# Optimization experiments

Measured on AMD Instinct MI355X. Metric: run time of the kernel, lower is better.

The kernel has to match this reference:

```python
import jax, jax.numpy as jnp
import numpy as np

B, IC, H, W = 32, 128, 112, 112
OC, K, STRIDE, PAD = 256, 3, 2, 1


def setup_inputs() -> dict:
    key = jax.random.key(0)
    kx, kw = jax.random.split(key)
    x = jax.random.normal(kx, (B, IC, H, W), dtype=jnp.float32)
    weight = jax.random.normal(kw, (OC, IC, K, K), dtype=jnp.float32) * 0.01
    bias = jnp.zeros((OC,), dtype=jnp.float32)
    return {"x": x, "weight": weight, "bias": bias}


def reference(x, weight, bias):
    # Equivalent of the nested-loop conv: standard cross-correlation,
    # stride=2, zero padding=1, NCHW / OIHW layouts.
    out = jax.lax.conv_general_dilated(
        x, weight,
        window_strides=(STRIDE, STRIDE),
        padding=[(PAD, PAD), (PAD, PAD)],
        dimension_numbers=("NCHW", "OIHW", "NCHW"),
    )
    return out + bias[None, :, None, None]
```

## Files before the change

kernel.cpp:

```cpp
#include <hip/hip_runtime.h>
#include <hip/hip_bf16.h>


#define B_    32
#define IC_   128
#define H_    112
#define W_    112
#define HW_   (H_ * W_)
#define OC_   256
#define HP    113
#define NPIX  (B_ * 56 * 56)
#define XT_BYTES ((size_t)B_ * HP * HP * IC_ * 2)
#define WT2_BYTES ((size_t)36 * 16384)

typedef __attribute__((ext_vector_type(8))) short bf16x8;
typedef __attribute__((ext_vector_type(4))) float f32x4;

static __device__ __forceinline__ unsigned f2bf_u(float f) {
  union { float f; unsigned u; } v; v.f = f;
  return (v.u + 0x7FFF + ((v.u >> 16) & 1)) >> 16;
}

__global__ __launch_bounds__(256) void xtrans_kernel(
    const float* __restrict__ x, unsigned short* __restrict__ xt) {
  __shared__ unsigned short lds[128 * 128];
  const int ihp = blockIdx.x;
  const int b   = blockIdx.y;
  const int tid = threadIdx.x;

  if (ihp > 0) {
    const float* xp = x + (size_t)b * IC_ * HW_ + (size_t)(ihp - 1) * W_;
#pragma unroll
    for (int it = 0; it < 16; ++it) {
      const int i  = tid + it * 256;
      const int ic = i >> 5;
      const int g  = i & 31;
      if (g < 28) {
        const float4 v = *reinterpret_cast<const float4*>(
            xp + (size_t)ic * HW_ + g * 4);
        uint2 p;
        p.x = f2bf_u(v.x) | (f2bf_u(v.y) << 16);
        p.y = f2bf_u(v.z) | (f2bf_u(v.w) << 16);
        const int gs = g ^ (((ic >> 3) & 7) << 2);
        *reinterpret_cast<uint2*>(&lds[ic * 128 + gs * 4]) = p;
      }
    }
  }
  __syncthreads();

  unsigned short* xrow = xt + ((size_t)(b * HP + ihp)) * (HP * IC_);
  const bool live = (ihp > 0);
#pragma unroll
  for (int it = 0; it < 8; ++it) {
    const int e = tid + it * 256;
    if (e >= HP * 16) break;
    const int iwp = e >> 4;
    const int icg = e & 15;
    uint4 v = {0u, 0u, 0u, 0u};
    if (live && iwp > 0) {
      const int iw  = iwp - 1;
      const int col = ((iw >> 2) ^ ((icg & 7) << 2)) * 4 + (iw & 3);
      const int r0  = icg * 8;
      unsigned u0 = lds[(r0 + 0) * 128 + col];
      unsigned u1 = lds[(r0 + 1) * 128 + col];
      unsigned u2 = lds[(r0 + 2) * 128 + col];
      unsigned u3 = lds[(r0 + 3) * 128 + col];
      unsigned u4 = lds[(r0 + 4) * 128 + col];
      unsigned u5 = lds[(r0 + 5) * 128 + col];
      unsigned u6 = lds[(r0 + 6) * 128 + col];
      unsigned u7 = lds[(r0 + 7) * 128 + col];
      v.x = u0 | (u1 << 16);
      v.y = u2 | (u3 << 16);
      v.z = u4 | (u5 << 16);
      v.w = u6 | (u7 << 16);
    }
    *reinterpret_cast<uint4*>(xrow + iwp * IC_ + icg * 8) = v;
  }
}

__global__ __launch_bounds__(256) void wtrans2_kernel(
    const float* __restrict__ w, unsigned short* __restrict__ wt2) {
  const int t  = blockIdx.x * 256 + threadIdx.x;
  const int oc = t >> 7;
  const int ic = t & 127;
  const int icc = ic >> 5, q = (ic >> 3) & 3, e = ic & 7;
  const float* ws = w + (size_t)t * 9;
#pragma unroll
  for (int tap = 0; tap < 9; ++tap) {
    const int step = tap * 4 + icc;
    wt2[((size_t)(step * 4 + q) * 256 + oc) * 8 + e] =
        (unsigned short)f2bf_u(ws[tap]);
  }
}

__global__ __launch_bounds__(256, 2) void conv_mfma_kernel(
    const unsigned short* __restrict__ xt, const unsigned short* __restrict__ wt2,
    const float* __restrict__ bias, float* __restrict__ out) {
  __shared__ unsigned short Wl[4][4096];
  __shared__ unsigned short Xl[4][4096];

  const int tid = threadIdx.x, wav = tid >> 6, lane = tid & 63;

  const int bid  = blockIdx.x;
  const int wgid = (bid & 7) * 196 + (bid >> 3);
  const int mt  = wgid & 1;
  const int pt  = wgid >> 1;
  const int oc0 = mt * 128;
  const int p0  = pt * 128;

  const char* xsrc[2];
#pragma unroll
  for (int i = 0; i < 2; ++i) {
    const int pix = p0 + i * 64 + lane;
    const int b   = pix / 3136;
    const int q   = pix - b * 3136;
    const int oh  = q / 56;
    const int ow  = q - oh * 56;
    const size_t e = (((size_t)b * HP + 2 * oh) * HP + 2 * ow) * IC_;
    xsrc[i] = reinterpret_cast<const char*>(xt) + e * 2 + wav * 16;
  }
  const char* wbase = reinterpret_cast<const char*>(wt2)
                    + wav * 4096 + mt * 2048 + lane * 16;

  auto stage = [&](int s, int buf) {
    const int tap = s >> 2, icc = s & 3;
    const int kh = tap / 3, kw = tap - kh * 3;
    const size_t xoff = ((size_t)(kh * HP + kw) * IC_ + icc * 32) * 2;
    const char* wsrc = wbase + (size_t)s * 16384;
    char* xd = reinterpret_cast<char*>(&Xl[buf][0]) + wav * 2048;
    char* wd = reinterpret_cast<char*>(&Wl[buf][0]) + wav * 2048;
#pragma unroll
    for (int i = 0; i < 2; ++i) {
      __builtin_amdgcn_global_load_lds(
          (const __attribute__((address_space(1))) void*)(xsrc[i] + xoff),
          (__attribute__((address_space(3))) void*)(xd + i * 1024), 16, 0, 0);
      __builtin_amdgcn_global_load_lds(
          (const __attribute__((address_space(1))) void*)(wsrc + i * 1024),
          (__attribute__((address_space(3))) void*)(wd + i * 1024), 16, 0, 0);
    }
  };

  const int wm = wav >> 1, wn = wav & 1;
  const int l15 = lane & 15, lg = lane >> 4;

  f32x4 acc[4][4] = {};

  auto compute = [&](int buf) {
    bf16x8 af[4], bx[4];
    const unsigned short* wb  = &Wl[buf][0] + lg * 1024;
    const unsigned short* xb2 = &Xl[buf][0] + lg * 1024;
#pragma unroll
    for (int mi = 0; mi < 4; ++mi)
      af[mi] = *reinterpret_cast<const bf16x8*>(
          wb + (wm * 64 + mi * 16 + l15) * 8);
#pragma unroll
    for (int ni = 0; ni < 4; ++ni)
      bx[ni] = *reinterpret_cast<const bf16x8*>(
          xb2 + (wn * 64 + ni * 16 + l15) * 8);
#pragma unroll
    for (int mi = 0; mi < 4; ++mi)
#pragma unroll
      for (int ni = 0; ni < 4; ++ni)
        acc[mi][ni] = __builtin_amdgcn_mfma_f32_16x16x32_bf16(
            af[mi], bx[ni], acc[mi][ni], 0, 0, 0);
  };

#define FENCED_BARRIER()                          \
  __builtin_amdgcn_sched_barrier(0);              \
  __builtin_amdgcn_s_barrier();                   \
  __builtin_amdgcn_sched_barrier(0)

  stage(0, 0);
  stage(1, 1);
  asm volatile("s_waitcnt vmcnt(4)" ::: "memory");
  FENCED_BARRIER();

  for (int s = 0; s < 34; ++s) {
    stage(s + 2, (s + 2) & 3);
    asm volatile("s_waitcnt vmcnt(8)" ::: "memory");
    FENCED_BARRIER();
    compute(s & 3);
  }
  asm volatile("s_waitcnt vmcnt(4)" ::: "memory");
  FENCED_BARRIER();
  compute(34 & 3);
  asm volatile("s_waitcnt vmcnt(0)" ::: "memory");
  FENCED_BARRIER();
  compute(35 & 3);
#undef FENCED_BARRIER

#pragma unroll
  for (int mi = 0; mi < 4; ++mi) {
#pragma unroll
    for (int j = 0; j < 4; ++j) {
      const int oc = oc0 + wm * 64 + mi * 16 + lg * 4 + j;
      const float bv = bias[oc];
#pragma unroll
      for (int ni = 0; ni < 4; ++ni) {
        const int pix = p0 + wn * 64 + ni * 16 + l15;
        const int b   = pix / 3136;
        const int q   = pix - b * 3136;
        out[((size_t)b * OC_ + oc) * 3136 + q] = acc[mi][ni][j] + bv;
      }
    }
  }
}

__global__ __launch_bounds__(256) void conv2d_f32_kernel(
    const float* __restrict__ x, const float* __restrict__ w,
    const float* __restrict__ bias, float* __restrict__ out) {
  __shared__ float wlds[IC_ * 9][8];
  const int b   = blockIdx.z;
  const int oc0 = blockIdx.y * 8;
  const float* wsrc = w + (size_t)oc0 * (IC_ * 9);
  for (int i = threadIdx.x; i < IC_ * 9 * 8; i += 256) {
    const int j = i / (IC_ * 9);
    const int t = i - j * (IC_ * 9);
    wlds[t][j] = wsrc[(size_t)j * (IC_ * 9) + t];
  }
  __syncthreads();
  const int p  = blockIdx.x * 256 + threadIdx.x;
  const int ow = p % 56;
  const int oh = p / 56;
  const bool pv = (oh < 56);
  const int ih0 = 2 * oh - 1;
  const int iw0 = 2 * ow - 1;
  const float* xb = x + (size_t)b * IC_ * HW_ + (ptrdiff_t)ih0 * W_ + iw0;
  float acc[8];
#pragma unroll
  for (int j = 0; j < 8; ++j) acc[j] = 0.f;
  for (int ic = 0; ic < IC_; ++ic) {
    const float* xc = xb + (size_t)ic * HW_;
#pragma unroll
    for (int kh = 0; kh < 3; ++kh) {
      const bool hv = pv && ((ih0 + kh) >= 0);
#pragma unroll
      for (int kw = 0; kw < 3; ++kw) {
        const bool v = hv && ((iw0 + kw) >= 0);
        const float xv = v ? xc[kh * W_ + kw] : 0.f;
        const int t = ic * 9 + kh * 3 + kw;
        const float4 w0 = *reinterpret_cast<const float4*>(&wlds[t][0]);
        const float4 w1 = *reinterpret_cast<const float4*>(&wlds[t][4]);
        acc[0] = fmaf(xv, w0.x, acc[0]); acc[1] = fmaf(xv, w0.y, acc[1]);
        acc[2] = fmaf(xv, w0.z, acc[2]); acc[3] = fmaf(xv, w0.w, acc[3]);
        acc[4] = fmaf(xv, w1.x, acc[4]); acc[5] = fmaf(xv, w1.y, acc[5]);
        acc[6] = fmaf(xv, w1.z, acc[6]); acc[7] = fmaf(xv, w1.w, acc[7]);
      }
    }
  }
  if (pv) {
#pragma unroll
    for (int j = 0; j < 8; ++j)
      out[(((size_t)(b * OC_ + oc0 + j)) * 56 + oh) * 56 + ow] =
          acc[j] + bias[oc0 + j];
  }
}

extern "C" void kernel_launch(void* const* d_in, const int* in_sizes, int n_in,
                              void* d_out, int out_size, void* d_ws, size_t ws_size,
                              hipStream_t stream) {
  const float* x    = (const float*)d_in[0];
  const float* w    = (const float*)d_in[1];
  const float* bias = (const float*)d_in[2];
  float* out        = (float*)d_out;

  if (ws_size >= XT_BYTES + WT2_BYTES) {
    unsigned short* xt  = (unsigned short*)d_ws;
    unsigned short* wt2 = (unsigned short*)((char*)d_ws + XT_BYTES);
    xtrans_kernel<<<dim3(HP, B_), 256, 0, stream>>>(x, xt);
    wtrans2_kernel<<<128, 256, 0, stream>>>(w, wt2);
    conv_mfma_kernel<<<NPIX / 64, 256, 0, stream>>>(xt, wt2, bias, out);
  } else {
    conv2d_f32_kernel<<<dim3(13, OC_ / 8, B_), 256, 0, stream>>>(x, w, bias, out);
  }
}
```

Baseline: 175.3 us.

## Switch to double-buffered LDS with repacked tile layout and simple syncthreads loop

Cuts the LDS ring from four stages to two and replaces the hand-tuned vmcnt waits and fenced barriers with a plain __syncthreads loop that issues the next stage before computing the current one. It also remaps which lanes load which weight and input rows, so each wave's MFMA operands sit in a contiguous LDS region. The launch bound's minimum-blocks hint is dropped. Smaller LDS may allow more resident blocks, but the shallower prefetch exposes more global-load latency. Correctness depends on __syncthreads waiting for the async global_load_lds writes, which is not explicit here.

```diff
diff --git a/kernel.cpp b/kernel.cpp
--- a/kernel.cpp
+++ b/kernel.cpp
@@ -93,11 +93,11 @@
   }
 }
 
-__global__ __launch_bounds__(256, 2) void conv_mfma_kernel(
+__global__ __launch_bounds__(256) void conv_mfma_kernel(
     const unsigned short* __restrict__ xt, const unsigned short* __restrict__ wt2,
     const float* __restrict__ bias, float* __restrict__ out) {
-  __shared__ unsigned short Wl[4][4096];
-  __shared__ unsigned short Xl[4][4096];
+  __shared__ unsigned short Wl[2][4096];
+  __shared__ unsigned short Xl[2][4096];
 
   const int tid = threadIdx.x, wav = tid >> 6, lane = tid & 63;
 
@@ -108,55 +108,62 @@
   const int oc0 = mt * 128;
   const int p0  = pt * 128;
 
+  const int l15 = lane & 15, lg = lane >> 4;
+
   const char* xsrc[2];
 #pragma unroll
   for (int i = 0; i < 2; ++i) {
-    const int pix = p0 + i * 64 + lane;
+    const int pix = p0 + (2 * wav + i) * 16 + l15;
     const int b   = pix / 3136;
     const int q   = pix - b * 3136;
     const int oh  = q / 56;
     const int ow  = q - oh * 56;
     const size_t e = (((size_t)b * HP + 2 * oh) * HP + 2 * ow) * IC_;
-    xsrc[i] = reinterpret_cast<const char*>(xt) + e * 2 + wav * 16;
-  }
-  const char* wbase = reinterpret_cast<const char*>(wt2)
-                    + wav * 4096 + mt * 2048 + lane * 16;
+    xsrc[i] = reinterpret_cast<const char*>(xt) + e * 2 + lg * 16;
+  }
+  const char* wsrc2[2];
+  int wdoff[2];
+#pragma unroll
+  for (int i = 0; i < 2; ++i) {
+    const int sh  = 2 * wav + i;
+    const int ocg = sh >> 2, qq = sh & 3;
+    wsrc2[i] = reinterpret_cast<const char*>(wt2)
+             + qq * 4096 + (oc0 + ocg * 64 + lane) * 16;
+    wdoff[i] = ocg * 4096 + qq * 1024;
+  }
 
   auto stage = [&](int s, int buf) {
     const int tap = s >> 2, icc = s & 3;
     const int kh = tap / 3, kw = tap - kh * 3;
     const size_t xoff = ((size_t)(kh * HP + kw) * IC_ + icc * 32) * 2;
-    const char* wsrc = wbase + (size_t)s * 16384;
+    const size_t woff = (size_t)s * 16384;
     char* xd = reinterpret_cast<char*>(&Xl[buf][0]) + wav * 2048;
-    char* wd = reinterpret_cast<char*>(&Wl[buf][0]) + wav * 2048;
+    char* wd = reinterpret_cast<char*>(&Wl[buf][0]);
 #pragma unroll
     for (int i = 0; i < 2; ++i) {
       __builtin_amdgcn_global_load_lds(
           (const __attribute__((address_space(1))) void*)(xsrc[i] + xoff),
           (__attribute__((address_space(3))) void*)(xd + i * 1024), 16, 0, 0);
       __builtin_amdgcn_global_load_lds(
-          (const __attribute__((address_space(1))) void*)(wsrc + i * 1024),
-          (__attribute__((address_space(3))) void*)(wd + i * 1024), 16, 0, 0);
+          (const __attribute__((address_space(1))) void*)(wsrc2[i] + woff),
+          (__attribute__((address_space(3))) void*)(wd + wdoff[i]), 16, 0, 0);
     }
   };
 
   const int wm = wav >> 1, wn = wav & 1;
-  const int l15 = lane & 15, lg = lane >> 4;
 
   f32x4 acc[4][4] = {};
 
   auto compute = [&](int buf) {
     bf16x8 af[4], bx[4];
-    const unsigned short* wb  = &Wl[buf][0] + lg * 1024;
-    const unsigned short* xb2 = &Xl[buf][0] + lg * 1024;
+    const unsigned short* wb  = &Wl[buf][0] + wm * 2048 + lg * 512;
+    const unsigned short* xb2 = &Xl[buf][0] + wn * 2048 + lg * 128;
 #pragma unroll
     for (int mi = 0; mi < 4; ++mi)
-      af[mi] = *reinterpret_cast<const bf16x8*>(
-          wb + (wm * 64 + mi * 16 + l15) * 8);
+      af[mi] = *reinterpret_cast<const bf16x8*>(wb + (mi * 16 + l15) * 8);
 #pragma unroll
     for (int ni = 0; ni < 4; ++ni)
-      bx[ni] = *reinterpret_cast<const bf16x8*>(
-          xb2 + (wn * 64 + ni * 16 + l15) * 8);
+      bx[ni] = *reinterpret_cast<const bf16x8*>(xb2 + ni * 512 + l15 * 8);
 #pragma unroll
     for (int mi = 0; mi < 4; ++mi)
 #pragma unroll
@@ -165,29 +172,13 @@
             af[mi], bx[ni], acc[mi][ni], 0, 0, 0);
   };
 
-#define FENCED_BARRIER()                          \
-  __builtin_amdgcn_sched_barrier(0);              \
-  __builtin_amdgcn_s_barrier();                   \
-  __builtin_amdgcn_sched_barrier(0)
-
   stage(0, 0);
-  stage(1, 1);
-  asm volatile("s_waitcnt vmcnt(4)" ::: "memory");
-  FENCED_BARRIER();
-
-  for (int s = 0; s < 34; ++s) {
-    stage(s + 2, (s + 2) & 3);
-    asm volatile("s_waitcnt vmcnt(8)" ::: "memory");
-    FENCED_BARRIER();
-    compute(s & 3);
-  }
-  asm volatile("s_waitcnt vmcnt(4)" ::: "memory");
-  FENCED_BARRIER();
-  compute(34 & 3);
-  asm volatile("s_waitcnt vmcnt(0)" ::: "memory");
-  FENCED_BARRIER();
-  compute(35 & 3);
-#undef FENCED_BARRIER
+  __syncthreads();
+  for (int s = 0; s < 36; ++s) {
+    if (s + 1 < 36) stage(s + 1, (s + 1) & 1);
+    compute(s & 1);
+    if (s + 1 < 36) __syncthreads();
+  }
 
 #pragma unroll
   for (int mi = 0; mi < 4; ++mi) {
```

After: 176.1 us. Within noise of the previous version (+0.5%).
